# Performance work log

Measured on AMD Instinct MI355X. Metric: run time of the kernel, lower is better.

Reference implementation:

```python
import jax, jax.numpy as jnp
import numpy as np

EMBED_DIM = 1024
NUM_HEADS = 16
ROTARY_THETA = 10000.0


def _rotate_half(t):
    d = t.shape[-1] // 2
    t1, t2 = t[..., :d], t[..., d:]
    return jnp.concatenate([-t2, t1], axis=-1)


def _rope_cos_sin(seq_len, head_dim, dtype):
    # inv_freq over even indices, standard RoPE
    inv_freq = 1.0 / (ROTARY_THETA ** (jnp.arange(0, head_dim, 2, dtype=jnp.float32) / head_dim))
    freqs = jnp.arange(seq_len, dtype=jnp.float32)[:, None] * inv_freq[None, :]  # (S, D/2)
    emb = jnp.concatenate([freqs, freqs], axis=-1)  # (S, D)
    # broadcast over (b, s, h, d)
    return jnp.cos(emb).astype(dtype)[None, :, None, :], jnp.sin(emb).astype(dtype)[None, :, None, :]


def setup_inputs() -> dict:
    key = jax.random.key(0)
    ks = jax.random.split(key, 4)
    B, S, E = 2, 2048, EMBED_DIM
    scale = 1.0 / np.sqrt(E)
    return {
        "x": jax.random.normal(ks[0], (B, S, E), dtype=jnp.float32),
        "attention_mask": jnp.zeros((B, 1, 1, S), dtype=jnp.float32),
        "Wq": jax.random.normal(ks[1], (E, E), dtype=jnp.float32) * scale,
        "bq": jnp.zeros((E,), dtype=jnp.float32),
        "Wk": jax.random.normal(ks[2], (E, E), dtype=jnp.float32) * scale,
        "bk": jnp.zeros((E,), dtype=jnp.float32),
        "Wv": jax.random.normal(ks[3], (E, E), dtype=jnp.float32) * scale,
        "bv": jnp.zeros((E,), dtype=jnp.float32),
    }


def reference(x, attention_mask, Wq, bq, Wk, bk, Wv, bv):
    B, S, E = x.shape
    H = NUM_HEADS
    D = E // H

    q = (x @ Wq + bq).reshape(B, S, H, D)
    k = (x @ Wk + bk).reshape(B, S, H, D)
    v = (x @ Wv + bv).reshape(B, S, H, D)

    cos, sin = _rope_cos_sin(S, D, q.dtype)
    q = q * cos + _rotate_half(q) * sin
    k = k * cos + _rotate_half(k) * sin

    # attention_mask: additive padding bias (b,1,1,k) broadcast over heads & queries
    scores = jnp.einsum("bqhd,bkhd->bhqk", q, k) / jnp.sqrt(jnp.asarray(D, dtype=q.dtype))
    scores = scores + attention_mask  # broadcasts to (b,h,q,k)
    attn = jax.nn.softmax(scores, axis=-1)
    out = jnp.einsum("bhqk,bkhd->bqhd", attn, v)
    return out.reshape(B, S, E)
```

## Files before the change

kernel.cpp:

```cpp
#include <hip/hip_runtime.h>

typedef __attribute__((ext_vector_type(8)))  short bf16x8;
typedef __attribute__((ext_vector_type(4)))  short s16x4;
typedef __attribute__((ext_vector_type(4)))  float f32x4;
typedef __attribute__((ext_vector_type(16))) float f32x16;
typedef __attribute__((ext_vector_type(4)))  unsigned u32x4;
typedef __attribute__((ext_vector_type(4)))  _Float16 f16x4;

#define B_  2
#define S_  2048
#define H_  16
#define D_  64
#define E_  1024
#define M_  (B_*S_)
#define NH_ (M_*H_)
#define L2E 1.44269504f

__device__ __forceinline__ unsigned short f2bf(float f){
  unsigned x = __builtin_bit_cast(unsigned, f);
  x += 0x7fffu + ((x >> 16) & 1u);
  return (unsigned short)(x >> 16);
}
__device__ __forceinline__ unsigned pk_bf16(float lo, float hi){
  unsigned short a = __builtin_bit_cast(unsigned short, (__bf16)lo);
  unsigned short b = __builtin_bit_cast(unsigned short, (__bf16)hi);
  return (unsigned)a | ((unsigned)b << 16);
}

#define GLD16(gp, lp) __builtin_amdgcn_global_load_lds( \
    (const __attribute__((address_space(1))) unsigned*)(gp), \
    (__attribute__((address_space(3))) unsigned*)(lp), 16, 0, 0)

__global__ __launch_bounds__(256) void k_prep(const float* __restrict__ in, short* __restrict__ out,
                                              const float* __restrict__ mask,
                                              float* ct, float* st, float* maskC,
                                              const float* __restrict__ Wq, const float* __restrict__ Wk,
                                              const float* __restrict__ Wv, short* __restrict__ wt){
  const int bx = blockIdx.x;
  if(bx < 4096){
    int i = bx*256 + threadIdx.x;
    if(i < S_*32){
      int s = i >> 5, f = i & 31;
      float invf = powf(10000.0f, -(float)f / 32.0f);
      float ph = (float)s * invf;
      ct[i] = cosf(ph);
      st[i] = sinf(ph);
      if(i < B_*S_) maskC[i] = fmaf(mask[i], L2E, -17.0f);
    }
    int j = i*4;
    float4 v = *(const float4*)(in + j);
    s16x4 o = { (short)f2bf(v.x), (short)f2bf(v.y), (short)f2bf(v.z), (short)f2bf(v.w) };
    *(s16x4*)(out + j) = o;
  } else {
    int w = bx - 4096;
    int z = w >> 8, r = w & 255;
    const float* W = z==0 ? Wq : (z==1 ? Wk : Wv);
    short* outw = wt + (size_t)z*E_*E_;
    __shared__ short tile[64][72];
    int nb = (r & 15)*64, kb = (r >> 4)*64;
    int t = threadIdx.x;
    {
      int rr = t>>2, c0 = (t&3)*16;
      const float* src = W + (size_t)(kb+rr)*E_ + nb + c0;
      #pragma unroll
      for(int i=0;i<4;i++){
        float4 v = *(const float4*)(src + i*4);
        tile[rr][c0+i*4+0] = (short)f2bf(v.x);
        tile[rr][c0+i*4+1] = (short)f2bf(v.y);
        tile[rr][c0+i*4+2] = (short)f2bf(v.z);
        tile[rr][c0+i*4+3] = (short)f2bf(v.w);
      }
    }
    __syncthreads();
    {
      int n = t>>2, k0 = (t&3)*16;
      short* dst = outw + (size_t)(nb+n)*E_ + kb + k0;
      bf16x8 o0, o1;
      #pragma unroll
      for(int i=0;i<8;i++){ o0[i] = tile[k0+i][n]; o1[i] = tile[k0+8+i][n]; }
      *(bf16x8*)dst = o0;
      *(bf16x8*)(dst+8) = o1;
    }
  }
}

__global__ __launch_bounds__(256) void k_gemm(const short* __restrict__ A, const short* __restrict__ WT,
                                              const float* __restrict__ biasq, const float* __restrict__ biask,
                                              const float* __restrict__ biasv,
                                              short* __restrict__ oq, short* __restrict__ ok, short* __restrict__ ovt,
                                              const float* __restrict__ cost, const float* __restrict__ sint){
  const int z = blockIdx.z;
  const short* Bw = WT + (size_t)z*E_*E_;
  const float* bias = z==0 ? biasq : (z==1 ? biask : biasv);
  __shared__ short As[128*64];
  __shared__ short Bs[128*64];
  const int t = threadIdx.x, lane = t & 63, wid = t >> 6;
  const int mb = blockIdx.x*128, nb = blockIdx.y*128;
  const int wm = (wid>>1)*64, wn = (wid&1)*64;
  f32x4 acc[4][4] = {};
  for(int kt=0; kt<E_/64; kt++){
    __syncthreads();
    #pragma unroll
    for(int i=0;i<4;i++){
      int c = t + 256*i;
      int row = c>>3;
      int colg = ((c&7) ^ (row&7))*8;
      GLD16(A  + (size_t)(mb + row)*E_ + kt*64 + colg, &As[c*8]);
      GLD16(Bw + (size_t)(nb + row)*E_ + kt*64 + colg, &Bs[c*8]);
    }
    __syncthreads();
    #pragma unroll
    for(int kk=0; kk<2; kk++){
      bf16x8 af[4], bfv[4];
      #pragma unroll
      for(int mf=0; mf<4; mf++){
        int r = wm + mf*16 + (lane&15);
        int c8 = (kk*4 + (lane>>4)) ^ (r&7);
        af[mf] = *(const bf16x8*)&As[r*64 + c8*8];
      }
      #pragma unroll
      for(int nf=0; nf<4; nf++){
        int r = wn + nf*16 + (lane&15);
        int c8 = (kk*4 + (lane>>4)) ^ (r&7);
        bfv[nf] = *(const bf16x8*)&Bs[r*64 + c8*8];
      }
      #pragma unroll
      for(int mf=0; mf<4; mf++)
        #pragma unroll
        for(int nf=0; nf<4; nf++)
          acc[mf][nf] = __builtin_amdgcn_mfma_f32_16x16x32_bf16(af[mf], bfv[nf], acc[mf][nf], 0, 0, 0);
    }
  }
  const int col16 = lane & 15, rg = lane >> 4;
  float bvs[4];
  #pragma unroll
  for(int nf=0; nf<4; nf++) bvs[nf] = bias[nb + wn + nf*16 + col16];
  if(z == 2){
    #pragma unroll
    for(int mf=0; mf<4; mf++){
      int row0 = mb + wm + mf*16 + rg*4;
      int bb2 = row0 >> 11, ss = row0 & (S_-1);
      #pragma unroll
      for(int nf=0; nf<4; nf++){
        int e = nb + wn + nf*16 + col16;
        int hh = e >> 6, dd = e & 63;
        s16x4 w = { (short)f2bf(acc[mf][nf][0]+bvs[nf]), (short)f2bf(acc[mf][nf][1]+bvs[nf]),
                    (short)f2bf(acc[mf][nf][2]+bvs[nf]), (short)f2bf(acc[mf][nf][3]+bvs[nf]) };
        *(s16x4*)(ovt + ((size_t)(bb2*H_+hh)*D_+dd)*S_ + ss) = w;
      }
    }
  } else {
    short* out = (z==0) ? oq : ok;
    const float qs = (z==0) ? (0.125f*L2E) : 1.0f;
    #pragma unroll
    for(int mf=0; mf<4; mf++)
      #pragma unroll
      for(int r=0; r<4; r++){
        int row = mb + wm + mf*16 + rg*4 + r;
        int srow = row & (S_-1);
        const float* cb = cost + (size_t)srow*32;
        const float* sb = sint + (size_t)srow*32;
        #pragma unroll
        for(int nf=0; nf<2; nf++){
          int d = nf*16 + col16;
          float c = cb[d], sn = sb[d];
          float x0 = acc[mf][nf][r]   + bvs[nf];
          float x1 = acc[mf][nf+2][r] + bvs[nf+2];
          out[(size_t)row*E_ + nb + wn + nf*16 + col16]     = (short)f2bf((x0*c - x1*sn)*qs);
          out[(size_t)row*E_ + nb + wn + (nf+2)*16 + col16] = (short)f2bf((x1*c + x0*sn)*qs);
        }
      }
  }
}

__global__ __launch_bounds__(256,4) void k_attn(
    const short* __restrict__ qg, const short* __restrict__ kg,
    const short* __restrict__ vtg, const float* __restrict__ maskC,
    float* __restrict__ o0g, _Float16* __restrict__ o1g, float* __restrict__ lpart){
  __shared__ short Ks[2][64*72];
  __shared__ short Vs[2][64*72];
  const int flat = blockIdx.x;
  const int v = flat >> 3;
  const int bh = (flat & 7)*4 + (v >> 5);
  const int inner = v & 31;
  const int qb = inner >> 1, sp = inner & 1;
  const int h = bh & 15, b = bh >> 4;
  const int tid = threadIdx.x, wid = tid>>6, lane = tid&63;
  const int l31 = lane & 31, hl = lane >> 5;
  const int qw = qb*128 + wid*32;
  const int rr = tid>>3, ch = tid&7;
  const int kb0 = sp*16;
  const int NT = 16;

  bf16x8 qf[4];
  {
    const short* qp = qg + ((size_t)(b*S_ + qw + l31)*H_ + h)*D_;
    #pragma unroll
    for(int dk=0; dk<4; dk++)
      qf[dk] = *(const bf16x8*)(qp + dk*16 + hl*8);
  }
  f32x16 O0 = {}, O1 = {};
  float l_run = 0.f;
  const float* mrow = maskC + (size_t)b*S_;

  bf16x8 ka, kc, va, vc;
#define LOADT(kb) { \
    const short* ks_ = kg + ((size_t)(b*S_ + (kb)*64 + rr)*H_ + h)*D_ + ch*8; \
    ka = *(const bf16x8*)ks_;  kc = *(const bf16x8*)(ks_ + 32*H_*D_); \
    const short* vs_ = vtg + ((size_t)(b*H_ + h)*D_ + rr)*S_ + (kb)*64 + ch*8; \
    va = *(const bf16x8*)vs_;  vc = *(const bf16x8*)(vs_ + 32*S_); }
#define WRITET(pp) { \
    *(bf16x8*)&Ks[pp][rr*72 + ch*8]      = ka; \
    *(bf16x8*)&Ks[pp][(rr+32)*72 + ch*8] = kc; \
    *(bf16x8*)&Vs[pp][rr*72 + ch*8]      = va; \
    *(bf16x8*)&Vs[pp][(rr+32)*72 + ch*8] = vc; }

  LOADT(kb0);
  WRITET(0);
  LOADT(kb0+1);
  asm volatile("s_waitcnt lgkmcnt(0)" ::: "memory");
  __builtin_amdgcn_s_barrier();

  int p = 0;
  for(int tt=0; tt<NT; tt++){
    f32x16 s0 = {}, s1 = {};
    __builtin_amdgcn_s_setprio(1);
    #pragma unroll
    for(int dk=0; dk<4; dk++){
      bf16x8 kf0 = *(const bf16x8*)&Ks[p][(l31)*72 + dk*16 + hl*8];
      bf16x8 kf1 = *(const bf16x8*)&Ks[p][(32+l31)*72 + dk*16 + hl*8];
      s0 = __builtin_amdgcn_mfma_f32_32x32x16_bf16(kf0, qf[dk], s0, 0,0,0);
      s1 = __builtin_amdgcn_mfma_f32_32x32x16_bf16(kf1, qf[dk], s1, 0,0,0);
    }
    __builtin_amdgcn_s_setprio(0);
    {
      const float* mt = mrow + (kb0+tt)*64 + hl*4;
      #pragma unroll
      for(int bb=0; bb<4; bb++){
        f32x4 mv0 = *(const f32x4*)(mt + bb*8);
        f32x4 mv1 = *(const f32x4*)(mt + 32 + bb*8);
        #pragma unroll
        for(int a=0; a<4; a++){ s0[bb*4+a] += mv0[a]; s1[bb*4+a] += mv1[a]; }
      }
    }
    #pragma unroll
    for(int i=0;i<16;i++) s0[i] = __builtin_amdgcn_exp2f(s0[i]);
    #pragma unroll
    for(int i=0;i<16;i++) s1[i] = __builtin_amdgcn_exp2f(s1[i]);
    float la=0.f, lb=0.f, lc=0.f, ld=0.f;
    #pragma unroll
    for(int i=0;i<4;i++){
      la += s0[i];   lb += s0[4+i];  lc += s0[8+i];  ld += s0[12+i];
      la += s1[i];   lb += s1[4+i];  lc += s1[8+i];  ld += s1[12+i];
    }
    float ls = (la+lb)+(lc+ld);
    ls += __shfl_xor(ls, 32);
    l_run += ls;

    unsigned w0a[8], w1a[8];
    #pragma unroll
    for(int c=0;c<8;c++){
      int base = (c&3)*4;
      float p0 = (c & 4) ? s1[base+0] : s0[base+0];
      float p1 = (c & 4) ? s1[base+1] : s0[base+1];
      float p2 = (c & 4) ? s1[base+2] : s0[base+2];
      float p3 = (c & 4) ? s1[base+3] : s0[base+3];
      w0a[c] = pk_bf16(p0, p1);
      w1a[c] = pk_bf16(p2, p3);
    }

    if(tt+1 < NT){
      WRITET(p^1);
      if(tt+2 < NT) LOADT(kb0+tt+2);
    }

    __builtin_amdgcn_s_setprio(1);
    #pragma unroll
    for(int ksl=0; ksl<4; ksl++){
      unsigned a0 = w0a[2*ksl], b0 = w0a[2*ksl+1];
      unsigned a1 = w1a[2*ksl], b1 = w1a[2*ksl+1];
      asm("v_permlane32_swap_b32 %0, %1" : "+v"(a0), "+v"(b0));
      asm("v_permlane32_swap_b32 %0, %1" : "+v"(a1), "+v"(b1));
      u32x4 pw = { a0, a1, b0, b1 };
      bf16x8 pf = __builtin_bit_cast(bf16x8, pw);
      bf16x8 vf0 = *(const bf16x8*)&Vs[p][(l31)*72 + ksl*16 + hl*8];
      bf16x8 vf1 = *(const bf16x8*)&Vs[p][(32+l31)*72 + ksl*16 + hl*8];
      O0 = __builtin_amdgcn_mfma_f32_32x32x16_bf16(pf, vf0, O0, 0,0,0);
      O1 = __builtin_amdgcn_mfma_f32_32x32x16_bf16(pf, vf1, O1, 0,0,0);
    }
    __builtin_amdgcn_s_setprio(0);
    asm volatile("s_waitcnt lgkmcnt(0)" ::: "memory");
    __builtin_amdgcn_s_barrier();
    p ^= 1;
  }
#undef LOADT
#undef WRITET

  if(sp == 0){
    #pragma unroll
    for(int bb=0; bb<4; bb++)
      #pragma unroll
      for(int a=0; a<4; a++){
        int qrow = qw + a + 8*bb + 4*hl;
        float* op = o0g + ((size_t)(b*S_ + qrow)*H_ + h)*D_;
        op[l31]      = O0[bb*4+a];
        op[32 + l31] = O1[bb*4+a];
      }
  } else {
    #pragma unroll
    for(int bb=0; bb<4; bb++)
      #pragma unroll
      for(int a=0; a<4; a++){
        int qrow = qw + a + 8*bb + 4*hl;
        _Float16* op = o1g + ((size_t)(b*S_ + qrow)*H_ + h)*D_;
        op[l31]      = (_Float16)O0[bb*4+a];
        op[32 + l31] = (_Float16)O1[bb*4+a];
      }
  }
  if(lane < 32)
    lpart[(size_t)sp*NH_ + (size_t)(b*S_ + qw + l31)*H_ + h] = l_run;
}

__global__ __launch_bounds__(256) void k_comb(float* __restrict__ out, const _Float16* __restrict__ o1,
                                              const float* __restrict__ lpart){
  int i = blockIdx.x*256 + threadIdx.x;
  int idx = i*4;
  int lidx = idx >> 6;
  float linv = 1.f / (lpart[lidx] + lpart[NH_ + lidx]);
  f32x4 a = *(f32x4*)(out + idx);
  f16x4 bb = *(const f16x4*)(o1 + idx);
  f32x4 r = { (a[0] + (float)bb[0])*linv, (a[1] + (float)bb[1])*linv,
              (a[2] + (float)bb[2])*linv, (a[3] + (float)bb[3])*linv };
  *(f32x4*)(out + idx) = r;
}

extern "C" void kernel_launch(void* const* d_in, const int* in_sizes, int n_in,
                              void* d_out, int out_size, void* d_ws, size_t ws_size,
                              hipStream_t stream){
  (void)in_sizes; (void)n_in; (void)out_size; (void)ws_size;
  const float* x    = (const float*)d_in[0];
  const float* mask = (const float*)d_in[1];
  const float* Wq   = (const float*)d_in[2];
  const float* bq   = (const float*)d_in[3];
  const float* Wk   = (const float*)d_in[4];
  const float* bk   = (const float*)d_in[5];
  const float* Wv   = (const float*)d_in[6];
  const float* bv   = (const float*)d_in[7];
  float* out = (float*)d_out;
  char* ws = (char*)d_ws;
  float* cost  = (float*)(ws);
  float* sint  = (float*)(ws + (256u<<10));
  float* maskC = (float*)(ws + (512u<<10));
  float* lpart = (float*)(ws + (768u<<10));
  short* xb    = (short*)(ws + (2u<<20));
  short* wt    = (short*)(ws + (10u<<20));
  short* qb    = (short*)(ws + (16u<<20));
  short* kb    = (short*)(ws + (24u<<20));
  short* vtb   = (short*)(ws + (32u<<20));
  _Float16* o1 = (_Float16*)xb;

  k_prep<<<dim3(4096+768), dim3(256), 0, stream>>>(x, xb, mask, cost, sint, maskC,
                                                   Wq, Wk, Wv, wt);
  k_gemm<<<dim3(32,8,3), dim3(256), 0, stream>>>(xb, wt, bq, bk, bv, qb, kb, vtb, cost, sint);
  k_attn<<<dim3(1024), dim3(256), 0, stream>>>(qb, kb, vtb, maskC, out, o1, lpart);
  k_comb<<<dim3(4096), dim3(256), 0, stream>>>(out, o1, lpart);
}
```

Baseline: 113.9 us.

## Split attention key range three ways with single-buffered LDS kernel variant

Adds a k_attn_s kernel that splits each query block's 32 key tiles across three blocks instead of two, giving 1536 blocks rather than 1024 for better CU fill. It uses single-buffered K/V LDS tiles with register prefetch and extra barriers. The combine kernel now sums a third fp16 partial and normalizer. The three-way path is taken only when the workspace is at least 48MB. Otherwise the old two-way path runs, so whether the new code executes depends on the harness workspace size.

```diff
diff --git a/kernel.cpp b/kernel.cpp
--- a/kernel.cpp
+++ b/kernel.cpp
@@ -172,6 +172,69 @@
       }
   }
 }
+
+#define ATTN_TILE_BODY(KS, VS, TTABS) \
+    f32x16 s0 = {}, s1 = {}; \
+    __builtin_amdgcn_s_setprio(1); \
+    _Pragma("unroll") \
+    for(int dk=0; dk<4; dk++){ \
+      bf16x8 kf0 = *(const bf16x8*)&KS[(l31)*72 + dk*16 + hl*8]; \
+      bf16x8 kf1 = *(const bf16x8*)&KS[(32+l31)*72 + dk*16 + hl*8]; \
+      s0 = __builtin_amdgcn_mfma_f32_32x32x16_bf16(kf0, qf[dk], s0, 0,0,0); \
+      s1 = __builtin_amdgcn_mfma_f32_32x32x16_bf16(kf1, qf[dk], s1, 0,0,0); \
+    } \
+    __builtin_amdgcn_s_setprio(0); \
+    { \
+      const float* mt = mrow + (TTABS)*64 + hl*4; \
+      _Pragma("unroll") \
+      for(int bb=0; bb<4; bb++){ \
+        f32x4 mv0 = *(const f32x4*)(mt + bb*8); \
+        f32x4 mv1 = *(const f32x4*)(mt + 32 + bb*8); \
+        _Pragma("unroll") \
+        for(int a=0; a<4; a++){ s0[bb*4+a] += mv0[a]; s1[bb*4+a] += mv1[a]; } \
+      } \
+    } \
+    _Pragma("unroll") \
+    for(int i=0;i<16;i++) s0[i] = __builtin_amdgcn_exp2f(s0[i]); \
+    _Pragma("unroll") \
+    for(int i=0;i<16;i++) s1[i] = __builtin_amdgcn_exp2f(s1[i]); \
+    float la=0.f, lb=0.f, lc=0.f, ld=0.f; \
+    _Pragma("unroll") \
+    for(int i=0;i<4;i++){ \
+      la += s0[i];   lb += s0[4+i];  lc += s0[8+i];  ld += s0[12+i]; \
+      la += s1[i];   lb += s1[4+i];  lc += s1[8+i];  ld += s1[12+i]; \
+    } \
+    float ls = (la+lb)+(lc+ld); \
+    ls += __shfl_xor(ls, 32); \
+    l_run += ls; \
+    unsigned w0a[8], w1a[8]; \
+    _Pragma("unroll") \
+    for(int c=0;c<8;c++){ \
+      int base = (c&3)*4; \
+      float p0 = (c & 4) ? s1[base+0] : s0[base+0]; \
+      float p1 = (c & 4) ? s1[base+1] : s0[base+1]; \
+      float p2 = (c & 4) ? s1[base+2] : s0[base+2]; \
+      float p3 = (c & 4) ? s1[base+3] : s0[base+3]; \
+      w0a[c] = pk_bf16(p0, p1); \
+      w1a[c] = pk_bf16(p2, p3); \
+    }
+
+#define ATTN_PV_BODY(VS) \
+    __builtin_amdgcn_s_setprio(1); \
+    _Pragma("unroll") \
+    for(int ksl=0; ksl<4; ksl++){ \
+      unsigned a0 = w0a[2*ksl], b0 = w0a[2*ksl+1]; \
+      unsigned a1 = w1a[2*ksl], b1 = w1a[2*ksl+1]; \
+      asm("v_permlane32_swap_b32 %0, %1" : "+v"(a0), "+v"(b0)); \
+      asm("v_permlane32_swap_b32 %0, %1" : "+v"(a1), "+v"(b1)); \
+      u32x4 pw = { a0, a1, b0, b1 }; \
+      bf16x8 pf = __builtin_bit_cast(bf16x8, pw); \
+      bf16x8 vf0 = *(const bf16x8*)&VS[(l31)*72 + ksl*16 + hl*8]; \
+      bf16x8 vf1 = *(const bf16x8*)&VS[(32+l31)*72 + ksl*16 + hl*8]; \
+      O0 = __builtin_amdgcn_mfma_f32_32x32x16_bf16(pf, vf0, O0, 0,0,0); \
+      O1 = __builtin_amdgcn_mfma_f32_32x32x16_bf16(pf, vf1, O1, 0,0,0); \
+    } \
+    __builtin_amdgcn_s_setprio(0);
 
 __global__ __launch_bounds__(256,4) void k_attn(
     const short* __restrict__ qg, const short* __restrict__ kg,
@@ -223,72 +286,12 @@
 
   int p = 0;
   for(int tt=0; tt<NT; tt++){
-    f32x16 s0 = {}, s1 = {};
-    __builtin_amdgcn_s_setprio(1);
-    #pragma unroll
-    for(int dk=0; dk<4; dk++){
-      bf16x8 kf0 = *(const bf16x8*)&Ks[p][(l31)*72 + dk*16 + hl*8];
-      bf16x8 kf1 = *(const bf16x8*)&Ks[p][(32+l31)*72 + dk*16 + hl*8];
-      s0 = __builtin_amdgcn_mfma_f32_32x32x16_bf16(kf0, qf[dk], s0, 0,0,0);
-      s1 = __builtin_amdgcn_mfma_f32_32x32x16_bf16(kf1, qf[dk], s1, 0,0,0);
-    }
-    __builtin_amdgcn_s_setprio(0);
-    {
-      const float* mt = mrow + (kb0+tt)*64 + hl*4;
-      #pragma unroll
-      for(int bb=0; bb<4; bb++){
-        f32x4 mv0 = *(const f32x4*)(mt + bb*8);
-        f32x4 mv1 = *(const f32x4*)(mt + 32 + bb*8);
-        #pragma unroll
-        for(int a=0; a<4; a++){ s0[bb*4+a] += mv0[a]; s1[bb*4+a] += mv1[a]; }
-      }
-    }
-    #pragma unroll
-    for(int i=0;i<16;i++) s0[i] = __builtin_amdgcn_exp2f(s0[i]);
-    #pragma unroll
-    for(int i=0;i<16;i++) s1[i] = __builtin_amdgcn_exp2f(s1[i]);
-    float la=0.f, lb=0.f, lc=0.f, ld=0.f;
-    #pragma unroll
-    for(int i=0;i<4;i++){
-      la += s0[i];   lb += s0[4+i];  lc += s0[8+i];  ld += s0[12+i];
-      la += s1[i];   lb += s1[4+i];  lc += s1[8+i];  ld += s1[12+i];
-    }
-    float ls = (la+lb)+(lc+ld);
-    ls += __shfl_xor(ls, 32);
-    l_run += ls;
-
-    unsigned w0a[8], w1a[8];
-    #pragma unroll
-    for(int c=0;c<8;c++){
-      int base = (c&3)*4;
-      float p0 = (c & 4) ? s1[base+0] : s0[base+0];
-      float p1 = (c & 4) ? s1[base+1] : s0[base+1];
-      float p2 = (c & 4) ? s1[base+2] : s0[base+2];
-      float p3 = (c & 4) ? s1[base+3] : s0[base+3];
-      w0a[c] = pk_bf16(p0, p1);
-      w1a[c] = pk_bf16(p2, p3);
-    }
-
+    ATTN_TILE_BODY(Ks[p], Vs[p], kb0+tt)
     if(tt+1 < NT){
       WRITET(p^1);
       if(tt+2 < NT) LOADT(kb0+tt+2);
     }
-
-    __builtin_amdgcn_s_setprio(1);
-    #pragma unroll
-    for(int ksl=0; ksl<4; ksl++){
-      unsigned a0 = w0a[2*ksl], b0 = w0a[2*ksl+1];
-      unsigned a1 = w1a[2*ksl], b1 = w1a[2*ksl+1];
-      asm("v_permlane32_swap_b32 %0, %1" : "+v"(a0), "+v"(b0));
-      asm("v_permlane32_swap_b32 %0, %1" : "+v"(a1), "+v"(b1));
-      u32x4 pw = { a0, a1, b0, b1 };
-      bf16x8 pf = __builtin_bit_cast(bf16x8, pw);
-      bf16x8 vf0 = *(const bf16x8*)&Vs[p][(l31)*72 + ksl*16 + hl*8];
-      bf16x8 vf1 = *(const bf16x8*)&Vs[p][(32+l31)*72 + ksl*16 + hl*8];
-      O0 = __builtin_amdgcn_mfma_f32_32x32x16_bf16(pf, vf0, O0, 0,0,0);
-      O1 = __builtin_amdgcn_mfma_f32_32x32x16_bf16(pf, vf1, O1, 0,0,0);
-    }
-    __builtin_amdgcn_s_setprio(0);
+    ATTN_PV_BODY(Vs[p])
     asm volatile("s_waitcnt lgkmcnt(0)" ::: "memory");
     __builtin_amdgcn_s_barrier();
     p ^= 1;
@@ -321,23 +324,120 @@
     lpart[(size_t)sp*NH_ + (size_t)(b*S_ + qw + l31)*H_ + h] = l_run;
 }
 
-__global__ __launch_bounds__(256) void k_comb(float* __restrict__ out, const _Float16* __restrict__ o1,
-                                              const float* __restrict__ lpart){
+__global__ __launch_bounds__(256,4) void k_attn_s(
+    const short* __restrict__ qg, const short* __restrict__ kg,
+    const short* __restrict__ vtg, const float* __restrict__ maskC,
+    float* __restrict__ o0g, _Float16* __restrict__ p1g, _Float16* __restrict__ p2g,
+    float* __restrict__ lpart){
+  __shared__ short Ks[64*72];
+  __shared__ short Vs[64*72];
+  const int flat = blockIdx.x;
+  const int v = flat >> 3;
+  const int bh = (flat & 7)*4 + v/48;
+  const int inner = v % 48;
+  const int qb = inner/3, sp = inner%3;
+  const int h = bh & 15, b = bh >> 4;
+  const int tid = threadIdx.x, wid = tid>>6, lane = tid&63;
+  const int l31 = lane & 31, hl = lane >> 5;
+  const int qw = qb*128 + wid*32;
+  const int rr = tid>>3, ch = tid&7;
+  const int kb0 = (sp*32)/3;
+  const int NT  = ((sp+1)*32)/3 - kb0;
+
+  bf16x8 qf[4];
+  {
+    const short* qp = qg + ((size_t)(b*S_ + qw + l31)*H_ + h)*D_;
+    #pragma unroll
+    for(int dk=0; dk<4; dk++)
+      qf[dk] = *(const bf16x8*)(qp + dk*16 + hl*8);
+  }
+  f32x16 O0 = {}, O1 = {};
+  float l_run = 0.f;
+  const float* mrow = maskC + (size_t)b*S_;
+
+  bf16x8 ka, kc, va, vc;
+#define LOADT(kb) { \
+    const short* ks_ = kg + ((size_t)(b*S_ + (kb)*64 + rr)*H_ + h)*D_ + ch*8; \
+    ka = *(const bf16x8*)ks_;  kc = *(const bf16x8*)(ks_ + 32*H_*D_); \
+    const short* vs_ = vtg + ((size_t)(b*H_ + h)*D_ + rr)*S_ + (kb)*64 + ch*8; \
+    va = *(const bf16x8*)vs_;  vc = *(const bf16x8*)(vs_ + 32*S_); }
+#define WRITET() { \
+    *(bf16x8*)&Ks[rr*72 + ch*8]      = ka; \
+    *(bf16x8*)&Ks[(rr+32)*72 + ch*8] = kc; \
+    *(bf16x8*)&Vs[rr*72 + ch*8]      = va; \
+    *(bf16x8*)&Vs[(rr+32)*72 + ch*8] = vc; }
+
+  LOADT(kb0);
+  WRITET();
+  __syncthreads();
+
+  for(int tt=0; tt<NT; tt++){
+    if(tt+1 < NT) LOADT(kb0+tt+1);
+    ATTN_TILE_BODY(Ks, Vs, kb0+tt)
+    ATTN_PV_BODY(Vs)
+    __syncthreads();
+    if(tt+1 < NT){
+      WRITET();
+      __syncthreads();
+    }
+  }
+#undef LOADT
+#undef WRITET
+
+  if(sp == 0){
+    #pragma unroll
+    for(int bb=0; bb<4; bb++)
+      #pragma unroll
+      for(int a=0; a<4; a++){
+        int qrow = qw + a + 8*bb + 4*hl;
+        float* op = o0g + ((size_t)(b*S_ + qrow)*H_ + h)*D_;
+        op[l31]      = O0[bb*4+a];
+        op[32 + l31] = O1[bb*4+a];
+      }
+  } else {
+    _Float16* pbuf = (sp == 1) ? p1g : p2g;
+    #pragma unroll
+    for(int bb=0; bb<4; bb++)
+      #pragma unroll
+      for(int a=0; a<4; a++){
+        int qrow = qw + a + 8*bb + 4*hl;
+        _Float16* op = pbuf + ((size_t)(b*S_ + qrow)*H_ + h)*D_;
+        op[l31]      = (_Float16)O0[bb*4+a];
+        op[32 + l31] = (_Float16)O1[bb*4+a];
+      }
+  }
+  if(lane < 32)
+    lpart[(size_t)sp*NH_ + (size_t)(b*S_ + qw + l31)*H_ + h] = l_run;
+}
+
+__global__ __launch_bounds__(256) void k_comb(float* __restrict__ out, const _Float16* __restrict__ p1,
+                                              const _Float16* __restrict__ p2,
+                                              const float* __restrict__ lpart, int ns){
   int i = blockIdx.x*256 + threadIdx.x;
   int idx = i*4;
   int lidx = idx >> 6;
-  float linv = 1.f / (lpart[lidx] + lpart[NH_ + lidx]);
+  float l = lpart[lidx] + lpart[NH_ + lidx];
+  if(ns > 2) l += lpart[2*NH_ + lidx];
+  float linv = 1.f / l;
   f32x4 a = *(f32x4*)(out + idx);
-  f16x4 bb = *(const f16x4*)(o1 + idx);
-  f32x4 r = { (a[0] + (float)bb[0])*linv, (a[1] + (float)bb[1])*linv,
-              (a[2] + (float)bb[2])*linv, (a[3] + (float)bb[3])*linv };
+  f16x4 q1 = *(const f16x4*)(p1 + idx);
+  f32x4 r;
+  #pragma unroll
+  for(int j=0;j<4;j++) r[j] = a[j] + (float)q1[j];
+  if(ns > 2){
+    f16x4 q2 = *(const f16x4*)(p2 + idx);
+    #pragma unroll
+    for(int j=0;j<4;j++) r[j] += (float)q2[j];
+  }
+  #pragma unroll
+  for(int j=0;j<4;j++) r[j] *= linv;
   *(f32x4*)(out + idx) = r;
 }
 
 extern "C" void kernel_launch(void* const* d_in, const int* in_sizes, int n_in,
                               void* d_out, int out_size, void* d_ws, size_t ws_size,
                               hipStream_t stream){
-  (void)in_sizes; (void)n_in; (void)out_size; (void)ws_size;
+  (void)in_sizes; (void)n_in; (void)out_size;
   const float* x    = (const float*)d_in[0];
   const float* mask = (const float*)d_in[1];
   const float* Wq   = (const float*)d_in[2];
@@ -357,11 +457,18 @@
   short* qb    = (short*)(ws + (16u<<20));
   short* kb    = (short*)(ws + (24u<<20));
   short* vtb   = (short*)(ws + (32u<<20));
-  _Float16* o1 = (_Float16*)xb;
+  _Float16* p1 = (_Float16*)xb;
+  _Float16* p2 = (_Float16*)(ws + (40u<<20));
+
+  const int ns = (ws_size >= (size_t)(48u<<20)) ? 3 : 2;
 
   k_prep<<<dim3(4096+768), dim3(256), 0, stream>>>(x, xb, mask, cost, sint, maskC,
                                                    Wq, Wk, Wv, wt);
   k_gemm<<<dim3(32,8,3), dim3(256), 0, stream>>>(xb, wt, bq, bk, bv, qb, kb, vtb, cost, sint);
-  k_attn<<<dim3(1024), dim3(256), 0, stream>>>(qb, kb, vtb, maskC, out, o1, lpart);
-  k_comb<<<dim3(4096), dim3(256), 0, stream>>>(out, o1, lpart);
-}
+  if(ns == 2){
+    k_attn<<<dim3(1024), dim3(256), 0, stream>>>(qb, kb, vtb, maskC, out, p1, lpart);
+  } else {
+    k_attn_s<<<dim3(1536), dim3(256), 0, stream>>>(qb, kb, vtb, maskC, out, p1, p2, lpart);
+  }
+  k_comb<<<dim3(4096), dim3(256), 0, stream>>>(out, p1, p2, lpart, ns);
+}
```

Measured after the change: 120.4 us. 1.06x slower.

## Enlarge QKV GEMM tiles to 256x256 with double-buffered LDS prefetch

Applied to the files above, without the earlier changes.

The QKV projection GEMM now uses 512-thread blocks computing 256x256 output tiles, with two LDS buffers. The next K-slice is fetched into the spare buffer while the current slice is consumed, in four phases with barriers and raised wave priority around the MFMA bursts. The goal is to overlap global loads with matrix math and to reuse each loaded tile across more output. In exchange the grid drops to 192 blocks, fewer than the number of CUs, and each block uses about 128KB of LDS, so occupancy and CU coverage go down.

```diff
diff --git a/kernel.cpp b/kernel.cpp
--- a/kernel.cpp
+++ b/kernel.cpp
@@ -84,7 +84,7 @@
   }
 }
 
-__global__ __launch_bounds__(256) void k_gemm(const short* __restrict__ A, const short* __restrict__ WT,
+__global__ __launch_bounds__(512,2) void k_gemm(const short* __restrict__ A, const short* __restrict__ WT,
                                               const float* __restrict__ biasq, const float* __restrict__ biask,
                                               const float* __restrict__ biasv,
                                               short* __restrict__ oq, short* __restrict__ ok, short* __restrict__ ovt,
@@ -92,57 +92,90 @@
   const int z = blockIdx.z;
   const short* Bw = WT + (size_t)z*E_*E_;
   const float* bias = z==0 ? biasq : (z==1 ? biask : biasv);
-  __shared__ short As[128*64];
-  __shared__ short Bs[128*64];
+  __shared__ short As[2][256*64];
+  __shared__ short Bs[2][256*64];
   const int t = threadIdx.x, lane = t & 63, wid = t >> 6;
-  const int mb = blockIdx.x*128, nb = blockIdx.y*128;
-  const int wm = (wid>>1)*64, wn = (wid&1)*64;
-  f32x4 acc[4][4] = {};
-  for(int kt=0; kt<E_/64; kt++){
+  const int wr = wid >> 2, wc = wid & 3;
+  const int mb = blockIdx.x*256, nb = blockIdx.y*256;
+  const int l15 = lane & 15, lq = lane >> 4;
+  f32x4 acc[8][4] = {};
+
+  #pragma unroll
+  for(int j=0;j<4;j++){
+    int c = t + 512*j;
+    int row = c>>3;
+    int colg = ((c&7) ^ (row&7))*8;
+    GLD16(A  + (size_t)(mb + row)*E_ + colg, &As[0][c*8]);
+    GLD16(Bw + (size_t)(nb + row)*E_ + colg, &Bs[0][c*8]);
+  }
+  __syncthreads();
+
+  for(int kt=0; kt<16; kt++){
+    const int cur = kt & 1;
+    const short* Asc = As[cur];
+    const short* Bsc = Bs[cur];
+    short* Asn = As[cur^1];
+    short* Bsn = Bs[cur^1];
+    const bool pf = (kt+1 < 16);
+    #pragma unroll
+    for(int ph=0; ph<4; ph++){
+      const int mq = ph>>1, nq = ph&1;
+      bf16x8 af[4][2], bf[2][2];
+      #pragma unroll
+      for(int i=0;i<4;i++){
+        int r = wr*128 + (mq*4+i)*16 + l15;
+        #pragma unroll
+        for(int kk=0;kk<2;kk++){
+          int c8 = (kk*4 + lq) ^ (r&7);
+          af[i][kk] = *(const bf16x8*)&Asc[r*64 + c8*8];
+        }
+      }
+      #pragma unroll
+      for(int j2=0;j2<2;j2++){
+        int r = wc*64 + (nq*2+j2)*16 + l15;
+        #pragma unroll
+        for(int kk=0;kk<2;kk++){
+          int c8 = (kk*4 + lq) ^ (r&7);
+          bf[j2][kk] = *(const bf16x8*)&Bsc[r*64 + c8*8];
+        }
+      }
+      if(pf){
+        int c = t + 512*ph;
+        int row = c>>3;
+        int colg = ((c&7) ^ (row&7))*8;
+        GLD16(A  + (size_t)(mb + row)*E_ + (kt+1)*64 + colg, &Asn[c*8]);
+        GLD16(Bw + (size_t)(nb + row)*E_ + (kt+1)*64 + colg, &Bsn[c*8]);
+      }
+      __builtin_amdgcn_s_barrier();
+      asm volatile("s_waitcnt lgkmcnt(0)" ::: "memory");
+      __builtin_amdgcn_sched_barrier(0);
+      __builtin_amdgcn_s_setprio(1);
+      #pragma unroll
+      for(int i=0;i<4;i++)
+        #pragma unroll
+        for(int j2=0;j2<2;j2++)
+          #pragma unroll
+          for(int kk=0;kk<2;kk++)
+            acc[mq*4+i][nq*2+j2] = __builtin_amdgcn_mfma_f32_16x16x32_bf16(
+                af[i][kk], bf[j2][kk], acc[mq*4+i][nq*2+j2], 0, 0, 0);
+      __builtin_amdgcn_s_setprio(0);
+      if(ph < 3) __builtin_amdgcn_s_barrier();
+    }
     __syncthreads();
-    #pragma unroll
-    for(int i=0;i<4;i++){
-      int c = t + 256*i;
-      int row = c>>3;
-      int colg = ((c&7) ^ (row&7))*8;
-      GLD16(A  + (size_t)(mb + row)*E_ + kt*64 + colg, &As[c*8]);
-      GLD16(Bw + (size_t)(nb + row)*E_ + kt*64 + colg, &Bs[c*8]);
-    }
-    __syncthreads();
-    #pragma unroll
-    for(int kk=0; kk<2; kk++){
-      bf16x8 af[4], bfv[4];
-      #pragma unroll
-      for(int mf=0; mf<4; mf++){
-        int r = wm + mf*16 + (lane&15);
-        int c8 = (kk*4 + (lane>>4)) ^ (r&7);
-        af[mf] = *(const bf16x8*)&As[r*64 + c8*8];
-      }
-      #pragma unroll
-      for(int nf=0; nf<4; nf++){
-        int r = wn + nf*16 + (lane&15);
-        int c8 = (kk*4 + (lane>>4)) ^ (r&7);
-        bfv[nf] = *(const bf16x8*)&Bs[r*64 + c8*8];
-      }
-      #pragma unroll
-      for(int mf=0; mf<4; mf++)
-        #pragma unroll
-        for(int nf=0; nf<4; nf++)
-          acc[mf][nf] = __builtin_amdgcn_mfma_f32_16x16x32_bf16(af[mf], bfv[nf], acc[mf][nf], 0, 0, 0);
-    }
-  }
-  const int col16 = lane & 15, rg = lane >> 4;
+  }
+
+  const int col16 = l15, rg = lq;
   float bvs[4];
   #pragma unroll
-  for(int nf=0; nf<4; nf++) bvs[nf] = bias[nb + wn + nf*16 + col16];
+  for(int nf=0; nf<4; nf++) bvs[nf] = bias[nb + wc*64 + nf*16 + col16];
   if(z == 2){
     #pragma unroll
-    for(int mf=0; mf<4; mf++){
-      int row0 = mb + wm + mf*16 + rg*4;
+    for(int mf=0; mf<8; mf++){
+      int row0 = mb + wr*128 + mf*16 + rg*4;
       int bb2 = row0 >> 11, ss = row0 & (S_-1);
       #pragma unroll
       for(int nf=0; nf<4; nf++){
-        int e = nb + wn + nf*16 + col16;
+        int e = nb + wc*64 + nf*16 + col16;
         int hh = e >> 6, dd = e & 63;
         s16x4 w = { (short)f2bf(acc[mf][nf][0]+bvs[nf]), (short)f2bf(acc[mf][nf][1]+bvs[nf]),
                     (short)f2bf(acc[mf][nf][2]+bvs[nf]), (short)f2bf(acc[mf][nf][3]+bvs[nf]) };
@@ -153,10 +186,10 @@
     short* out = (z==0) ? oq : ok;
     const float qs = (z==0) ? (0.125f*L2E) : 1.0f;
     #pragma unroll
-    for(int mf=0; mf<4; mf++)
+    for(int mf=0; mf<8; mf++)
       #pragma unroll
       for(int r=0; r<4; r++){
-        int row = mb + wm + mf*16 + rg*4 + r;
+        int row = mb + wr*128 + mf*16 + rg*4 + r;
         int srow = row & (S_-1);
         const float* cb = cost + (size_t)srow*32;
         const float* sb = sint + (size_t)srow*32;
@@ -166,8 +199,8 @@
           float c = cb[d], sn = sb[d];
           float x0 = acc[mf][nf][r]   + bvs[nf];
           float x1 = acc[mf][nf+2][r] + bvs[nf+2];
-          out[(size_t)row*E_ + nb + wn + nf*16 + col16]     = (short)f2bf((x0*c - x1*sn)*qs);
-          out[(size_t)row*E_ + nb + wn + (nf+2)*16 + col16] = (short)f2bf((x1*c + x0*sn)*qs);
+          out[(size_t)row*E_ + nb + wc*64 + nf*16 + col16]     = (short)f2bf((x0*c - x1*sn)*qs);
+          out[(size_t)row*E_ + nb + wc*64 + (nf+2)*16 + col16] = (short)f2bf((x1*c + x0*sn)*qs);
         }
       }
   }
@@ -361,7 +394,7 @@
 
   k_prep<<<dim3(4096+768), dim3(256), 0, stream>>>(x, xb, mask, cost, sint, maskC,
                                                    Wq, Wk, Wv, wt);
-  k_gemm<<<dim3(32,8,3), dim3(256), 0, stream>>>(xb, wt, bq, bk, bv, qb, kb, vtb, cost, sint);
+  k_gemm<<<dim3(16,4,3), dim3(512), 0, stream>>>(xb, wt, bq, bk, bv, qb, kb, vtb, cost, sint);
   k_attn<<<dim3(1024), dim3(256), 0, stream>>>(qb, kb, vtb, maskC, out, o1, lpart);
   k_comb<<<dim3(4096), dim3(256), 0, stream>>>(out, o1, lpart);
 }
```

New measurement: 111.8 us. Within noise of the previous version (-1.8%).
